# Kernel tuning notes

Hardware: AMD Instinct MI355X
Metric: run time of the kernel (lower is better)

## Reference

```python
import jax, jax.numpy as jnp
import numpy as np

B, H, W, C = 32, 56, 56, 384
NH, WS, SS = 12, 7, 3
DH = C // NH
N = WS * WS
HID = 4 * C
SCALE = DH ** -0.5


def _make_attn_mask(h, w, ws, ss):
    img = np.zeros((h, w), dtype=np.float32)
    cnt = 0
    for hs in (slice(0, -ws), slice(-ws, -ss), slice(-ss, None)):
        for wsl in (slice(0, -ws), slice(-ws, -ss), slice(-ss, None)):
            img[hs, wsl] = cnt
            cnt += 1
    mw = img.reshape(h // ws, ws, w // ws, ws).transpose(0, 2, 1, 3).reshape(-1, ws * ws)
    diff = mw[:, None, :] - mw[:, :, None]  # (nW, n, n)
    return np.where(diff != 0, np.float32(-100.0), np.float32(0.0))


def _make_rel_pos_index(ws):
    coords = np.stack(np.meshgrid(np.arange(ws), np.arange(ws), indexing='ij')).reshape(2, -1)
    rel = (coords[:, :, None] - coords[:, None, :]).transpose(1, 2, 0)  # (n, n, 2)
    rel[..., 0] += ws - 1
    rel[..., 1] += ws - 1
    rel[..., 0] *= 2 * ws - 1
    return rel.sum(-1)  # (n, n)


ATTN_MASK = jnp.asarray(_make_attn_mask(H, W, WS, SS))          # (nW, n, n)
REL_IDX = jnp.asarray(_make_rel_pos_index(WS))                   # (n, n)


def layernorm(x, g, b, eps):
    mu = jnp.mean(x, axis=-1, keepdims=True)
    var = jnp.var(x, axis=-1, keepdims=True)
    return (x - mu) * jax.lax.rsqrt(var + eps) * g + b


def window_partition(x, ws):
    b, h, w, c = x.shape
    x = x.reshape(b, h // ws, ws, w // ws, ws, c)
    return x.transpose(0, 1, 3, 2, 4, 5).reshape(-1, ws, ws, c)


def window_reverse(windows, ws, h, w):
    b = windows.shape[0] // ((h // ws) * (w // ws))
    x = windows.reshape(b, h // ws, w // ws, ws, ws, -1)
    return x.transpose(0, 1, 3, 2, 4, 5).reshape(b, h, w, -1)


def setup_inputs() -> dict:
    key = jax.random.key(0)
    ks = jax.random.split(key, 8)
    d = {
        'x': jax.random.normal(ks[0], (B, H * W, C), dtype=jnp.float32),
        'ln1_g': jnp.ones((C,), jnp.float32), 'ln1_b': jnp.zeros((C,), jnp.float32),
        'qkv_w': jax.random.normal(ks[1], (C, 3 * C), jnp.float32) * 0.02,
        'qkv_b': jnp.zeros((3 * C,), jnp.float32),
        'proj_w': jax.random.normal(ks[2], (C, C), jnp.float32) * 0.02,
        'proj_b': jnp.zeros((C,), jnp.float32),
        'rpb_table': jax.random.normal(ks[3], ((2 * WS - 1) ** 2, NH), jnp.float32) * 0.02,
        'ln2_g': jnp.ones((C,), jnp.float32), 'ln2_b': jnp.zeros((C,), jnp.float32),
        'ffln_g': jnp.ones((C,), jnp.float32), 'ffln_b': jnp.zeros((C,), jnp.float32),
        'ff1_w': jax.random.normal(ks[4], (C, HID), jnp.float32) * 0.02,
        'ff1_b': jnp.zeros((HID,), jnp.float32),
        'ff2_w': jax.random.normal(ks[5], (HID, C), jnp.float32) * 0.02,
        'ff2_b': jnp.zeros((C,), jnp.float32),
    }
    return d


def reference(x, ln1_g, ln1_b, qkv_w, qkv_b, proj_w, proj_b, rpb_table,
              ln2_g, ln2_b, ffln_g, ffln_b, ff1_w, ff1_b, ff2_w, ff2_b):
    b = x.shape[0]
    shortcut = x
    xn = layernorm(x, ln1_g, ln1_b, 1e-5).reshape(b, H, W, C)
    shifted = jnp.roll(xn, shift=(-SS, -SS), axis=(1, 2))
    xw = window_partition(shifted, WS).reshape(-1, N, C)  # (b*nW, n, c)
    Bw = xw.shape[0]
    nW = Bw // b

    qkv = (xw @ qkv_w + qkv_b).reshape(Bw, N, 3, NH, DH).transpose(2, 0, 3, 1, 4)
    q, k, v = qkv[0], qkv[1], qkv[2]  # (Bw, nh, n, dh)
    dots = jnp.einsum('bhnd,bhmd->bhnm', q, k) * SCALE

    bias = rpb_table[REL_IDX.reshape(-1)].reshape(N, N, NH).transpose(2, 0, 1)  # (nh, n, n)
    attn = dots + bias[None]
    attn = attn.reshape(b, nW, NH, N, N) + ATTN_MASK[None, :, None, :, :]
    attn = jax.nn.softmax(attn.reshape(Bw, NH, N, N), axis=-1)

    out = jnp.einsum('bhnm,bhmd->bhnd', attn, v)
    out = out.transpose(0, 2, 1, 3).reshape(Bw, N, C)
    out = out @ proj_w + proj_b

    out = window_reverse(out.reshape(-1, WS, WS, C), WS, H, W)
    out = jnp.roll(out, shift=(SS, SS), axis=(1, 2)).reshape(b, H * W, C)

    x = shortcut + out
    y = layernorm(x, ln2_g, ln2_b, 1e-5)
    y = layernorm(y, ffln_g, ffln_b, 1e-6)
    y = jax.nn.gelu(y @ ff1_w + ff1_b, approximate=False) @ ff2_w + ff2_b
    return x + y
```

## Files before the change

kernel.cpp:

```cpp
#include <hip/hip_runtime.h>
#include <hip/hip_bf16.h>

typedef short bf16x8 __attribute__((ext_vector_type(8)));
typedef short short4v __attribute__((ext_vector_type(4)));
typedef float f32x4  __attribute__((ext_vector_type(4)));

static constexpr float SCALE = 0.17677669529663687f;

__device__ __forceinline__ void gload_lds16(const void* g, void* l) {
  __builtin_amdgcn_global_load_lds(
      (const __attribute__((address_space(1))) unsigned int*)g,
      (__attribute__((address_space(3))) unsigned int*)l, 16, 0, 0);
}

__device__ __forceinline__ size_t win_to_nat(int t) {
  int win = t / 49; int n = t - win * 49;
  int bb = win >> 6; int wimg = win & 63;
  int hb = wimg >> 3, wb = wimg & 7;
  int nr = n / 7, nc = n - nr * 7;
  int hh = hb * 7 + nr + 3; if (hh >= 56) hh -= 56;
  int ww = wb * 7 + nc + 3; if (ww >= 56) ww -= 56;
  return (size_t)bb * 3136 + (size_t)hh * 56 + ww;
}

__device__ __forceinline__ float gelu_fast(float x) {
  float t = __expf(-1.702f * x);
  return x / (1.f + t);
}

__global__ __launch_bounds__(256)
void k_transpose(const float* __restrict__ W, __hip_bfloat16* __restrict__ Wt,
                 int K, int N) {
  __shared__ float tile[32][33];
  int tx = threadIdx.x & 31, ty = threadIdx.x >> 5;
  int tc = blockIdx.x, tr = blockIdx.y;
#pragma unroll
  for (int r = 0; r < 32; r += 8)
    tile[r + ty][tx] = W[(size_t)(tr * 32 + r + ty) * N + tc * 32 + tx];
  __syncthreads();
#pragma unroll
  for (int r = 0; r < 32; r += 8)
    Wt[(size_t)(tc * 32 + r + ty) * K + tr * 32 + tx] =
        __float2bfloat16(tile[tx][r + ty]);
}

__global__ __launch_bounds__(256)
void k_ln1(const float* __restrict__ x, const float* __restrict__ gw,
           const float* __restrict__ bw, __hip_bfloat16* __restrict__ xw) {
  int lane = threadIdx.x & 63;
  int t = blockIdx.x * 4 + (threadIdx.x >> 6);
  size_t nt = win_to_nat(t);
  const float* xr = x + nt * 384;
  float4 a  = *(const float4*)(xr + lane * 4);
  float2 c2 = *(const float2*)(xr + 256 + lane * 2);
  float v[6] = {a.x, a.y, a.z, a.w, c2.x, c2.y};
  int c0 = lane * 4, c1 = 256 + lane * 2;
  int ch[6] = {c0, c0 + 1, c0 + 2, c0 + 3, c1, c1 + 1};
  float s = 0.f, q = 0.f;
#pragma unroll
  for (int i = 0; i < 6; i++) { s += v[i]; q += v[i] * v[i]; }
#pragma unroll
  for (int m = 1; m < 64; m <<= 1) { s += __shfl_xor(s, m); q += __shfl_xor(q, m); }
  float mean = s * (1.f / 384.f);
  float rstd = rsqrtf(q * (1.f / 384.f) - mean * mean + 1e-5f);
  __hip_bfloat16* o = xw + (size_t)t * 384;
#pragma unroll
  for (int i = 0; i < 6; i++)
    o[ch[i]] = __float2bfloat16((v[i] - mean) * rstd * gw[ch[i]] + bw[ch[i]]);
}

__global__ __launch_bounds__(256)
void k_ln2ff(const float* __restrict__ xres, const float* __restrict__ g2,
             const float* __restrict__ b2, const float* __restrict__ gf,
             const float* __restrict__ bf_, __hip_bfloat16* __restrict__ yln) {
  int lane = threadIdx.x & 63;
  int t = blockIdx.x * 4 + (threadIdx.x >> 6);
  const float* xr = xres + (size_t)t * 384;
  float4 a  = *(const float4*)(xr + lane * 4);
  float2 c2 = *(const float2*)(xr + 256 + lane * 2);
  float v[6] = {a.x, a.y, a.z, a.w, c2.x, c2.y};
  int c0 = lane * 4, c1 = 256 + lane * 2;
  int ch[6] = {c0, c0 + 1, c0 + 2, c0 + 3, c1, c1 + 1};
  float s = 0.f, q = 0.f;
#pragma unroll
  for (int i = 0; i < 6; i++) { s += v[i]; q += v[i] * v[i]; }
#pragma unroll
  for (int m = 1; m < 64; m <<= 1) { s += __shfl_xor(s, m); q += __shfl_xor(q, m); }
  float mean = s * (1.f / 384.f);
  float rstd = rsqrtf(q * (1.f / 384.f) - mean * mean + 1e-5f);
  float y1[6];
  s = 0.f; q = 0.f;
#pragma unroll
  for (int i = 0; i < 6; i++) {
    y1[i] = (v[i] - mean) * rstd * g2[ch[i]] + b2[ch[i]];
    s += y1[i]; q += y1[i] * y1[i];
  }
#pragma unroll
  for (int m = 1; m < 64; m <<= 1) { s += __shfl_xor(s, m); q += __shfl_xor(q, m); }
  float m2 = s * (1.f / 384.f);
  float r2 = rsqrtf(q * (1.f / 384.f) - m2 * m2 + 1e-6f);
  __hip_bfloat16* o = yln + (size_t)t * 384;
#pragma unroll
  for (int i = 0; i < 6; i++)
    o[ch[i]] = __float2bfloat16((y1[i] - m2) * r2 * gf[ch[i]] + bf_[ch[i]]);
}

enum { EPI_QKV = 0, EPI_PROJ = 1, EPI_FF1 = 2, EPI_FF2 = 3 };

template <int EPI>
__global__ __launch_bounds__(256)
void k_gemm(const __hip_bfloat16* __restrict__ A, const __hip_bfloat16* __restrict__ Wt,
            const float* __restrict__ bias, int K, int nCol, int cpx,
            const float* __restrict__ aux,
            float* __restrict__ out_f,
            __hip_bfloat16* __restrict__ out_b) {
  __shared__ __hip_bfloat16 LB[16384];
  int tid = threadIdx.x;
  int lane = tid & 63, w = tid >> 6;
  int g = lane >> 4, r16 = lane & 15;
  int wr = w >> 1, wc = w & 1;

  int bid = blockIdx.x;
  int wg = (bid & 7) * cpx + (bid >> 3);
  int rB = wg / nCol;
  int rowBlk = rB * 128;
  int colBlk = (wg - rB * nCol) * 128;

  int srow = tid >> 2;
  int cch = (tid & 3) ^ (srow & 3);
  const __hip_bfloat16* PA = A + (size_t)(rowBlk + srow) * K + cch * 8;
  const __hip_bfloat16* PB = Wt + (size_t)(colBlk + srow) * K + cch * 8;

#define STG(NB, T)                                                            \
  {                                                                           \
    int k0s = (T) << 5;                                                       \
    _Pragma("unroll") for (int j = 0; j < 2; j++) {                           \
      gload_lds16(PA + (size_t)j * 64 * K + k0s, &LB[(NB) * 4096 + j * 2048 + w * 512]); \
      gload_lds16(PB + (size_t)j * 64 * K + k0s, &LB[8192 + (NB) * 4096 + j * 2048 + w * 512]); \
    }                                                                         \
  }

  int aBase = (wr * 64 + r16) * 32;
  int bBase = 8192 + (wc * 64 + r16) * 32;
  int sw = (g ^ (r16 & 3)) * 8;

  f32x4 acc[4][4] = {};
  const int nt = K >> 5;

  STG(0, 0)

  for (int t = 0; t < nt; ++t) {
    int cur = t & 1;
    if (t + 1 < nt) {
      STG(cur ^ 1, t + 1)
      asm volatile("s_waitcnt vmcnt(4)" ::: "memory");
    } else {
      asm volatile("s_waitcnt vmcnt(0)" ::: "memory");
    }
    __builtin_amdgcn_s_barrier();

    bf16x8 a[4], b[4];
#pragma unroll
    for (int mi = 0; mi < 4; mi++)
      a[mi] = *(const bf16x8*)(&LB[cur * 4096 + aBase + mi * 512 + sw]);
#pragma unroll
    for (int ni = 0; ni < 4; ni++)
      b[ni] = *(const bf16x8*)(&LB[cur * 4096 + bBase + ni * 512 + sw]);
    __builtin_amdgcn_s_setprio(1);
#pragma unroll
    for (int mi = 0; mi < 4; mi++)
#pragma unroll
      for (int ni = 0; ni < 4; ni++)
        acc[mi][ni] = __builtin_amdgcn_mfma_f32_16x16x32_bf16(b[ni], a[mi], acc[mi][ni], 0, 0, 0);
    __builtin_amdgcn_s_setprio(0);
    __builtin_amdgcn_s_barrier();
  }
#undef STG

  if constexpr (EPI == EPI_QKV || EPI == EPI_FF1) {
    __hip_bfloat16* EP = &LB[w * 4096];
#pragma unroll
    for (int ni = 0; ni < 4; ni++) {
      float4 b4 = *(const float4*)(bias + colBlk + wc * 64 + ni * 16 + g * 4);
#pragma unroll
      for (int mi = 0; mi < 4; mi++) {
        float v0 = acc[mi][ni][0] + b4.x, v1 = acc[mi][ni][1] + b4.y,
              v2 = acc[mi][ni][2] + b4.z, v3 = acc[mi][ni][3] + b4.w;
        if constexpr (EPI == EPI_FF1) {
          v0 = gelu_fast(v0); v1 = gelu_fast(v1);
          v2 = gelu_fast(v2); v3 = gelu_fast(v3);
        }
        short4v s4 = {(short)__bfloat16_as_ushort(__float2bfloat16(v0)),
                      (short)__bfloat16_as_ushort(__float2bfloat16(v1)),
                      (short)__bfloat16_as_ushort(__float2bfloat16(v2)),
                      (short)__bfloat16_as_ushort(__float2bfloat16(v3))};
        int row = mi * 16 + r16;
        int ch8 = (ni * 2 + (g >> 1)) ^ (row & 7);
        *(short4v*)(&EP[row * 64 + ch8 * 8 + (g & 1) * 4]) = s4;
      }
    }
#pragma unroll
    for (int j = 0; j < 8; j++) {
      int r = j * 8 + (lane >> 3);
      bf16x8 vv = *(const bf16x8*)(&EP[r * 64 + ((lane & 7) ^ (r & 7)) * 8]);
      int grow = rowBlk + wr * 64 + r;
      int col0 = colBlk + wc * 64 + (lane & 7) * 8;
      if constexpr (EPI == EPI_QKV) {
        int winr = grow / 49, nn = grow - winr * 49;
        int which = col0 / 384; int rem = col0 - which * 384;
        int hh = rem >> 5, dd = rem & 31;
        size_t off = (((size_t)winr * 12 + hh) * 49 + nn) * 32 + dd;
        *(bf16x8*)(out_b + (size_t)which * 38535168u + off) = vv;
      } else {
        *(bf16x8*)(out_b + (size_t)grow * 1536 + col0) = vv;
      }
    }
  } else {
    float* EPF = (float*)LB + w * 2048;
#pragma unroll
    for (int half = 0; half < 2; half++) {
#pragma unroll
      for (int ni = 0; ni < 4; ni++) {
        float4 b4 = *(const float4*)(bias + colBlk + wc * 64 + ni * 16 + g * 4);
#pragma unroll
        for (int mi2 = 0; mi2 < 2; mi2++) {
          int mi = half * 2 + mi2;
          f32x4 v = acc[mi][ni];
          v[0] += b4.x; v[1] += b4.y; v[2] += b4.z; v[3] += b4.w;
          int row = mi2 * 16 + r16;
          int ch4 = (ni * 4 + g) ^ r16;
          *(f32x4*)(&EPF[row * 64 + ch4 * 4]) = v;
        }
      }
#pragma unroll
      for (int j = 0; j < 8; j++) {
        int r = j * 4 + g;
        f32x4 vv = *(const f32x4*)(&EPF[r * 64 + ((r16 ^ (r & 15)) * 4)]);
        int grow = rowBlk + wr * 64 + half * 32 + r;
        int col0 = colBlk + wc * 64 + r16 * 4;
        if constexpr (EPI == EPI_PROJ) {
          size_t nt2 = win_to_nat(grow);
          const float4 a4 = *(const float4*)(aux + nt2 * 384 + col0);
          float4 o4 = {vv[0] + a4.x, vv[1] + a4.y, vv[2] + a4.z, vv[3] + a4.w};
          *(float4*)(out_f + nt2 * 384 + col0) = o4;
        } else {
          const float4 a4 = *(const float4*)(aux + (size_t)grow * 384 + col0);
          float4 o4 = {vv[0] + a4.x, vv[1] + a4.y, vv[2] + a4.z, vv[3] + a4.w};
          *(float4*)(out_f + (size_t)grow * 384 + col0) = o4;
        }
      }
    }
  }
}

__global__ __launch_bounds__(256)
void k_attn(const __hip_bfloat16* __restrict__ q, const __hip_bfloat16* __restrict__ k,
            const __hip_bfloat16* __restrict__ v, const float* __restrict__ rpb,
            __hip_bfloat16* __restrict__ o) {
  __shared__ __hip_bfloat16 P[4][64][72];
  int tid = threadIdx.x;
  int lane = tid & 63, wave = tid >> 6;
  int g = lane >> 4, r16 = lane & 15;
  int gid = blockIdx.x * 4 + wave;
  int wi = gid / 12, h = gid - (gid / 12) * 12;
  int wimg = wi & 63;
  int hb = wimg >> 3, wb = wimg & 7;
  size_t base = ((size_t)wi * 12 + h) * (49 * 32);
  const __hip_bfloat16* qb = q + base;
  const __hip_bfloat16* kb = k + base;
  const __hip_bfloat16* vb = v + base;

  bf16x8 zf = {0, 0, 0, 0, 0, 0, 0, 0};
  bf16x8 qf[4], kf[4];
#pragma unroll
  for (int mi = 0; mi < 4; mi++) {
    int row = mi * 16 + r16;
    qf[mi] = (row < 49) ? *(const bf16x8*)(qb + row * 32 + g * 8) : zf;
    kf[mi] = (row < 49) ? *(const bf16x8*)(kb + row * 32 + g * 8) : zf;
  }
  f32x4 fz = {0.f, 0.f, 0.f, 0.f};
  f32x4 S[4][4];
#pragma unroll
  for (int mi = 0; mi < 4; mi++)
#pragma unroll
    for (int ni = 0; ni < 4; ni++)
      S[mi][ni] = __builtin_amdgcn_mfma_f32_16x16x32_bf16(qf[mi], kf[ni], fz, 0, 0, 0);

  int kiA[4], kjA[4], rkA[4], cvA[4];
#pragma unroll
  for (int ni = 0; ni < 4; ni++) {
    int col = ni * 16 + r16;
    cvA[ni] = (col < 49);
    int ki = col / 7, kj = col - (col / 7) * 7;
    kiA[ni] = ki; kjA[ni] = kj;
    int hg = hb * 7 + ki, wg = wb * 7 + kj;
    int rh = (hg < 49) ? 0 : ((hg < 53) ? 1 : 2);
    int rw = (wg < 49) ? 0 : ((wg < 53) ? 1 : 2);
    rkA[ni] = rh * 3 + rw;
  }

#pragma unroll
  for (int mi = 0; mi < 4; mi++) {
#pragma unroll
    for (int rr = 0; rr < 4; rr++) {
      int row = mi * 16 + g * 4 + rr;
      float sv[4];
      float mx = -1e30f;
      int qi = row / 7, qj = row - (row / 7) * 7;
      int hgq = hb * 7 + qi, wgq = wb * 7 + qj;
      int rhq = (hgq < 49) ? 0 : ((hgq < 53) ? 1 : 2);
      int rwq = (wgq < 49) ? 0 : ((wgq < 53) ? 1 : 2);
      int rq = rhq * 3 + rwq;
#pragma unroll
      for (int ni = 0; ni < 4; ni++) {
        float s = -1e30f;
        if (row < 49 && cvA[ni]) {
          int idx = (qi - kiA[ni] + 6) * 13 + (qj - kjA[ni] + 6);
          float maskv = (rq != rkA[ni]) ? -100.f : 0.f;
          s = S[mi][ni][rr] * SCALE + rpb[idx * 12 + h] + maskv;
        }
        sv[ni] = s;
        mx = fmaxf(mx, s);
      }
#pragma unroll
      for (int m = 1; m <= 8; m <<= 1) mx = fmaxf(mx, __shfl_xor(mx, m));
      float sum = 0.f;
#pragma unroll
      for (int ni = 0; ni < 4; ni++) {
        float p = __expf(sv[ni] - mx);
        sv[ni] = p; sum += p;
      }
#pragma unroll
      for (int m = 1; m <= 8; m <<= 1) sum += __shfl_xor(sum, m);
      float inv = 1.f / sum;
#pragma unroll
      for (int ni = 0; ni < 4; ni++)
        P[wave][row][ni * 16 + r16] = __float2bfloat16(sv[ni] * inv);
    }
  }

  f32x4 O[4][2] = {};
#pragma unroll
  for (int ks = 0; ks < 2; ks++) {
    bf16x8 pf[4];
#pragma unroll
    for (int mi = 0; mi < 4; mi++)
      pf[mi] = *(const bf16x8*)(&P[wave][mi * 16 + r16][ks * 32 + g * 8]);
#pragma unroll
    for (int ni = 0; ni < 2; ni++) {
      bf16x8 vf = zf;
#pragma unroll
      for (int j = 0; j < 8; j++) {
        int m = ks * 32 + g * 8 + j;
        if (m < 49) vf[j] = ((const short*)vb)[m * 32 + ni * 16 + r16];
      }
#pragma unroll
      for (int mi = 0; mi < 4; mi++)
        O[mi][ni] = __builtin_amdgcn_mfma_f32_16x16x32_bf16(pf[mi], vf, O[mi][ni], 0, 0, 0);
    }
  }

#pragma unroll
  for (int mi = 0; mi < 4; mi++)
#pragma unroll
    for (int rr = 0; rr < 4; rr++) {
      int row = mi * 16 + g * 4 + rr;
      if (row < 49) {
#pragma unroll
        for (int ni = 0; ni < 2; ni++) {
          int col = ni * 16 + r16;
          o[(((size_t)wi * 49 + row) * 12 + h) * 32 + col] = __float2bfloat16(O[mi][ni][rr]);
        }
      }
    }
}

extern "C" void kernel_launch(void* const* d_in, const int* in_sizes, int n_in,
                              void* d_out, int out_size, void* d_ws, size_t ws_size,
                              hipStream_t stream) {
  const float* x      = (const float*)d_in[0];
  const float* ln1_g  = (const float*)d_in[1];
  const float* ln1_b  = (const float*)d_in[2];
  const float* qkv_w  = (const float*)d_in[3];
  const float* qkv_b  = (const float*)d_in[4];
  const float* proj_w = (const float*)d_in[5];
  const float* proj_b = (const float*)d_in[6];
  const float* rpb    = (const float*)d_in[7];
  const float* ln2_g  = (const float*)d_in[8];
  const float* ln2_b  = (const float*)d_in[9];
  const float* ffg    = (const float*)d_in[10];
  const float* ffb    = (const float*)d_in[11];
  const float* ff1_w  = (const float*)d_in[12];
  const float* ff1_b  = (const float*)d_in[13];
  const float* ff2_w  = (const float*)d_in[14];
  const float* ff2_b  = (const float*)d_in[15];
  float* out = (float*)d_out;

  char* ws = (char*)d_ws;
  __hip_bfloat16* xw     = (__hip_bfloat16*)ws;
  __hip_bfloat16* qbuf   = (__hip_bfloat16*)(ws + 77070336u);
  __hip_bfloat16* kbuf   = qbuf + 38535168u;
  __hip_bfloat16* vbuf   = kbuf + 38535168u;
  __hip_bfloat16* attn_o = xw;
  __hip_bfloat16* hbuf   = (__hip_bfloat16*)ws;
  float*          x_res  = (float*)(ws + 308281344u);
  __hip_bfloat16* yln    = (__hip_bfloat16*)(ws + 462422016u);
  __hip_bfloat16* qkv_wt = (__hip_bfloat16*)(ws + 539492352u);
  __hip_bfloat16* proj_wt = qkv_wt + 442368u;
  __hip_bfloat16* ff1_wt  = proj_wt + 147456u;
  __hip_bfloat16* ff2_wt  = ff1_wt + 589824u;

  k_transpose<<<dim3(1152 / 32, 384 / 32), dim3(256), 0, stream>>>(qkv_w, qkv_wt, 384, 1152);
  k_transpose<<<dim3(384 / 32, 384 / 32), dim3(256), 0, stream>>>(proj_w, proj_wt, 384, 384);
  k_transpose<<<dim3(1536 / 32, 384 / 32), dim3(256), 0, stream>>>(ff1_w, ff1_wt, 384, 1536);
  k_transpose<<<dim3(384 / 32, 1536 / 32), dim3(256), 0, stream>>>(ff2_w, ff2_wt, 1536, 384);

  k_ln1<<<dim3(25088), dim3(256), 0, stream>>>(x, ln1_g, ln1_b, xw);

  k_gemm<EPI_QKV><<<dim3(7056), dim3(256), 0, stream>>>(xw, qkv_wt, qkv_b, 384, 9, 7056 / 8,
                                                        nullptr, nullptr, qbuf);
  k_attn<<<dim3(6144), dim3(256), 0, stream>>>(qbuf, kbuf, vbuf, rpb, attn_o);
  k_gemm<EPI_PROJ><<<dim3(2352), dim3(256), 0, stream>>>(attn_o, proj_wt, proj_b, 384, 3, 2352 / 8,
                                                         x, x_res, nullptr);
  k_ln2ff<<<dim3(25088), dim3(256), 0, stream>>>(x_res, ln2_g, ln2_b, ffg, ffb, yln);
  k_gemm<EPI_FF1><<<dim3(9408), dim3(256), 0, stream>>>(yln, ff1_wt, ff1_b, 384, 12, 9408 / 8,
                                                        nullptr, nullptr, hbuf);
  k_gemm<EPI_FF2><<<dim3(2352), dim3(256), 0, stream>>>(hbuf, ff2_wt, ff2_b, 1536, 3, 2352 / 8,
                                                        x_res, out, nullptr);
}
```

Baseline: 934.1 us.

## Triple-buffer GEMM K-tiles and use an 8-slot XOR LDS swizzle

Grows the GEMM shared buffer from two to three K-tile stages so each tile is prefetched two steps ahead. Waitcnt thresholds are adjusted and the main loop is unrolled by three with rotating buffer indices. The LDS layout moves to a 64-element row pairing with an 8-way XOR swizzle, meant to reduce bank conflicts on the fragment reads. In exchange, LDS per block grows to 48KB, which can lower occupancy. The unroll also assumes K/32 is a multiple of three, which holds for K=384 and K=1536.

```diff
diff --git a/kernel.cpp b/kernel.cpp
--- a/kernel.cpp
+++ b/kernel.cpp
@@ -114,7 +114,7 @@
             const float* __restrict__ aux,
             float* __restrict__ out_f,
             __hip_bfloat16* __restrict__ out_b) {
-  __shared__ __hip_bfloat16 LB[16384];
+  __shared__ __hip_bfloat16 LB[24576];
   int tid = threadIdx.x;
   int lane = tid & 63, w = tid >> 6;
   int g = lane >> 4, r16 = lane & 15;
@@ -126,8 +126,9 @@
   int rowBlk = rB * 128;
   int colBlk = (wg - rB * nCol) * 128;
 
-  int srow = tid >> 2;
-  int cch = (tid & 3) ^ (srow & 3);
+  int s2 = (tid & 7) ^ ((tid >> 3) & 7);
+  int srow = 2 * (tid >> 3) + (s2 >> 2);
+  int cch = s2 & 3;
   const __hip_bfloat16* PA = A + (size_t)(rowBlk + srow) * K + cch * 8;
   const __hip_bfloat16* PB = Wt + (size_t)(colBlk + srow) * K + cch * 8;
 
@@ -136,45 +137,51 @@
     int k0s = (T) << 5;                                                       \
     _Pragma("unroll") for (int j = 0; j < 2; j++) {                           \
       gload_lds16(PA + (size_t)j * 64 * K + k0s, &LB[(NB) * 4096 + j * 2048 + w * 512]); \
-      gload_lds16(PB + (size_t)j * 64 * K + k0s, &LB[8192 + (NB) * 4096 + j * 2048 + w * 512]); \
+      gload_lds16(PB + (size_t)j * 64 * K + k0s, &LB[12288 + (NB) * 4096 + j * 2048 + w * 512]); \
     }                                                                         \
   }
 
-  int aBase = (wr * 64 + r16) * 32;
-  int bBase = 8192 + (wc * 64 + r16) * 32;
-  int sw = (g ^ (r16 & 3)) * 8;
+  int rslot = (g + ((r16 & 1) << 2)) ^ (r16 >> 1);
+  int aBase = (wr * 32 + (r16 >> 1)) * 64 + rslot * 8;
+  int bBase = 12288 + (wc * 32 + (r16 >> 1)) * 64 + rslot * 8;
 
   f32x4 acc[4][4] = {};
   const int nt = K >> 5;
 
   STG(0, 0)
-
-  for (int t = 0; t < nt; ++t) {
-    int cur = t & 1;
-    if (t + 1 < nt) {
-      STG(cur ^ 1, t + 1)
-      asm volatile("s_waitcnt vmcnt(4)" ::: "memory");
-    } else {
-      asm volatile("s_waitcnt vmcnt(0)" ::: "memory");
-    }
-    __builtin_amdgcn_s_barrier();
-
-    bf16x8 a[4], b[4];
-#pragma unroll
-    for (int mi = 0; mi < 4; mi++)
-      a[mi] = *(const bf16x8*)(&LB[cur * 4096 + aBase + mi * 512 + sw]);
-#pragma unroll
-    for (int ni = 0; ni < 4; ni++)
-      b[ni] = *(const bf16x8*)(&LB[cur * 4096 + bBase + ni * 512 + sw]);
-    __builtin_amdgcn_s_setprio(1);
-#pragma unroll
-    for (int mi = 0; mi < 4; mi++)
-#pragma unroll
-      for (int ni = 0; ni < 4; ni++)
-        acc[mi][ni] = __builtin_amdgcn_mfma_f32_16x16x32_bf16(b[ni], a[mi], acc[mi][ni], 0, 0, 0);
-    __builtin_amdgcn_s_setprio(0);
-    __builtin_amdgcn_s_barrier();
-  }
+  STG(1, 1)
+
+#define STEP(CB, SB, T)                                                       \
+  {                                                                           \
+    if ((T) + 2 < nt) {                                                       \
+      STG(SB, (T) + 2)                                                        \
+      asm volatile("s_waitcnt vmcnt(8)" ::: "memory");                        \
+    } else if ((T) + 1 < nt) {                                                \
+      asm volatile("s_waitcnt vmcnt(4)" ::: "memory");                        \
+    } else {                                                                  \
+      asm volatile("s_waitcnt vmcnt(0)" ::: "memory");                        \
+    }                                                                         \
+    __builtin_amdgcn_s_barrier();                \
+    bf16x8 a[4], b[4];                                                        \
+    _Pragma("unroll") for (int mi = 0; mi < 4; mi++)                          \
+      a[mi] = *(const bf16x8*)(&LB[(CB) * 4096 + aBase + mi * 512]);          \
+    _Pragma("unroll") for (int ni = 0; ni < 4; ni++)                          \
+      b[ni] = *(const bf16x8*)(&LB[(CB) * 4096 + bBase + ni * 512]);          \
+    __builtin_amdgcn_s_setprio(1);                                            \
+    _Pragma("unroll") for (int mi = 0; mi < 4; mi++)                          \
+      _Pragma("unroll") for (int ni = 0; ni < 4; ni++)                        \
+        acc[mi][ni] = __builtin_amdgcn_mfma_f32_16x16x32_bf16(                \
+            b[ni], a[mi], acc[mi][ni], 0, 0, 0);                              \
+    __builtin_amdgcn_s_setprio(0);                                            \
+    __builtin_amdgcn_s_barrier();     \
+  }
+
+  for (int t = 0; t < nt; t += 3) {
+    STEP(0, 2, t)
+    STEP(1, 0, t + 1)
+    STEP(2, 1, t + 2)
+  }
+#undef STEP
 #undef STG
 
   if constexpr (EPI == EPI_QKV || EPI == EPI_FF1) {
```

Measured after the change: 901.0 us. -3.6%, faster.
